# Optimization experiments

Hardware: AMD Instinct MI355X
Metric: run time of the kernel (lower is better)

The kernel has to match this reference:

```python
import jax, jax.numpy as jnp
import numpy as np

B, S, D = 1, 2048, 3072
H, DH = 24, 128
ENC, NIP = 512, 64
COND = (512 // 8) * (512 // 8) * 16 // 64  # 1024 cond tokens per lora
RANK, ALPHA, LW, IP_SCALE = 16, 16.0, 1.0, 1.0
EPS = 1e-5


def _rms(x):
    return x * jax.lax.rsqrt(jnp.mean(x * x, axis=-1, keepdims=True) + EPS)


def _to_heads(x):
    b, s, _ = x.shape
    return x.reshape(b, s, H, DH).transpose(0, 2, 1, 3)  # [B,H,S,DH]


def _from_heads(x):
    b, h, s, d = x.shape
    return x.transpose(0, 2, 1, 3).reshape(b, s, h * d)


def _lora(x, dn, up):
    # token mask keeps only the cond block (number=0, n_loras=1 -> last COND tokens)
    y = ((x[:, -COND:, :] @ dn) @ up) * (ALPHA / RANK)
    z = jnp.zeros((x.shape[0], x.shape[1] - COND, up.shape[1]), x.dtype)
    return jnp.concatenate([z, y], axis=1)


def _sdpa(q, k, v, mask=None):
    s = jnp.einsum('bhqd,bhkd->bhqk', q, k) * (1.0 / np.sqrt(DH))
    if mask is not None:
        s = s + mask
    return jnp.einsum('bhqk,bhkd->bhqd', jax.nn.softmax(s, axis=-1), v)


def _forward(hidden_states, encoder_hidden_states, image_emb,
             Wq, bq, Wk, bk, Wv, bv, Waq, baq, Wak, bak, Wav, bav,
             Wo, bo, Wao, bao, Wkip, Wvip,
             lq_dn, lq_up, lk_dn, lk_up, lv_dn, lv_up, lp_dn, lp_up):
    hs, ehs, img = hidden_states, encoder_hidden_states, image_emb
    # context (encoder) projections + RMSNorm on q/k
    eq = _rms(_to_heads(ehs @ Waq + baq))
    ek = _rms(_to_heads(ehs @ Wak + bak))
    ev = _to_heads(ehs @ Wav + bav)
    # main-stream q/k/v with masked LoRA branches
    q = hs @ Wq + bq + LW * _lora(hs, lq_dn, lq_up)
    k = hs @ Wk + bk + LW * _lora(hs, lk_dn, lk_up)
    v = hs @ Wv + bv + LW * _lora(hs, lv_dn, lv_up)
    q = _rms(_to_heads(q))
    k = _rms(_to_heads(k))
    v = _to_heads(v)
    # IP-adapter branch: extra K/V from image_emb, norm_added_k is RMSNorm(128)
    kip = _rms(_to_heads(img @ Wkip))
    vip = _to_heads(img @ Wvip)
    ip_out = _from_heads(_sdpa(q, kip, vip))  # [B,S,D]
    # concat encoder stream ahead of main stream
    q = jnp.concatenate([eq, q], axis=2)
    k = jnp.concatenate([ek, k], axis=2)
    v = jnp.concatenate([ev, v], axis=2)
    SL = ENC + S
    SB = SL - COND  # scaled_block_size
    m = jnp.ones((SL, SL), jnp.float32)
    m = m.at[:SB, :].set(0.0)        # non-cond rows attend everywhere
    m = m.at[SB:, SB:].set(0.0)      # single cond block attends to itself (n_loras=1)
    mask = m * (-1e20)
    out = _from_heads(_sdpa(q, k, v, mask))  # [B,SL,D]
    enc_out = out[:, :ENC, :]
    main = out[:, ENC:, :] + IP_SCALE * ip_out
    main = main @ Wo + bo
    main = main + LW * _lora(main, lp_dn, lp_up)  # proj LoRA (to_out dropout=identity)
    enc_out = enc_out @ Wao + bao
    return jnp.concatenate([enc_out, main], axis=1)  # [B, ENC+S, D]


def setup_inputs():
    key = jax.random.key(0)
    ks = iter(jax.random.split(key, 40))
    w = lambda *sh: jax.random.normal(next(ks), sh, jnp.float32) * 0.02
    return dict(
        hidden_states=jax.random.normal(next(ks), (B, S, D), jnp.float32),
        encoder_hidden_states=jax.random.normal(next(ks), (B, ENC, D), jnp.float32),
        image_emb=jax.random.normal(next(ks), (B, NIP, D), jnp.float32),
        Wq=w(D, D), bq=w(D), Wk=w(D, D), bk=w(D), Wv=w(D, D), bv=w(D),
        Waq=w(D, D), baq=w(D), Wak=w(D, D), bak=w(D), Wav=w(D, D), bav=w(D),
        Wo=w(D, D), bo=w(D), Wao=w(D, D), bao=w(D),
        Wkip=w(D, D), Wvip=w(D, D),
        lq_dn=w(D, RANK), lq_up=w(RANK, D), lk_dn=w(D, RANK), lk_up=w(RANK, D),
        lv_dn=w(D, RANK), lv_up=w(RANK, D), lp_dn=w(D, RANK), lp_up=w(RANK, D),
    )


def reference(hidden_states, encoder_hidden_states, image_emb,
              Wq, bq, Wk, bk, Wv, bv, Waq, baq, Wak, bak, Wav, bav,
              Wo, bo, Wao, bao, Wkip, Wvip,
              lq_dn, lq_up, lk_dn, lk_up, lv_dn, lv_up, lp_dn, lp_up):
    return _forward(hidden_states, encoder_hidden_states, image_emb,
                    Wq, bq, Wk, bk, Wv, bv, Waq, baq, Wak, bak, Wav, bav,
                    Wo, bo, Wao, bao, Wkip, Wvip,
                    lq_dn, lq_up, lk_dn, lk_up, lv_dn, lv_up, lp_dn, lp_up)
```

## Files before the change

### kernel.cpp

```cpp
#include <hip/hip_runtime.h>

typedef unsigned short u16;
typedef short s16x8 __attribute__((ext_vector_type(8)));
typedef float f32x4 __attribute__((ext_vector_type(4)));
typedef const __attribute__((address_space(1))) unsigned int* as1_u32p;
typedef __attribute__((address_space(3))) unsigned int* as3_u32p;

static_assert(sizeof(s16x8) == 16, "");

struct alignas(8) U16x4 { u16 x, y, z, w; };

__device__ __forceinline__ u16 f2bf(float f) {
  union { float f; unsigned u; } c; c.f = f;
  return (u16)((c.u + 0x7fffu + ((c.u >> 16) & 1u)) >> 16);
}
__device__ __forceinline__ float bf2f(u16 h) {
  union { unsigned u; float f; } c; c.u = ((unsigned)h) << 16;
  return c.f;
}
__device__ __forceinline__ void async16(const void* g, void* l) {
  __builtin_amdgcn_global_load_lds((as1_u32p)g, (as3_u32p)l, 16, 0, 0);
}

__launch_bounds__(256)
__global__ void mega_prep(const float* __restrict__ Waq, const float* __restrict__ Wak,
                          const float* __restrict__ Wav, const float* __restrict__ Wq,
                          const float* __restrict__ Wk, const float* __restrict__ Wv,
                          u16* __restrict__ WTbE, u16* __restrict__ WTbM,
                          const float* __restrict__ Wo, const float* __restrict__ bo,
                          const float* __restrict__ lp_dn, float* __restrict__ Wod,
                          const float* __restrict__ d0, const float* __restrict__ d1,
                          const float* __restrict__ d2, float* __restrict__ tl,
                          const float* __restrict__ hs, u16* __restrict__ hsb,
                          const float* __restrict__ ehs, u16* __restrict__ ehsb,
                          const float* __restrict__ img, u16* __restrict__ imgb,
                          const float* __restrict__ baq, const float* __restrict__ bak,
                          const float* __restrict__ bav, const float* __restrict__ bq,
                          const float* __restrict__ bk, const float* __restrict__ bv,
                          float* __restrict__ bpk,
                          const float* __restrict__ u0, const float* __restrict__ u1,
                          const float* __restrict__ u2) {
  __shared__ char lmem[4352];
  const int b = blockIdx.x;
  if (b < 55296) {
    int mat = b / 9216, tile = b % 9216;
    const float* src = (mat == 0) ? Waq : (mat == 1) ? Wak : (mat == 2) ? Wav
                       : (mat == 3) ? Wq : (mat == 4) ? Wk : Wv;
    u16* dst = (mat < 3) ? WTbE + (long)mat * 3072 * 3072
                         : WTbM + (long)(mat - 3) * 3072 * 3136;
    const int ldd = (mat < 3) ? 3072 : 3136;
    float (*tile2)[33] = (float(*)[33])lmem;
    int k0 = (tile / 96) * 32, n0 = (tile % 96) * 32;
    int r = threadIdx.x >> 3, c4 = (threadIdx.x & 7) * 4;
    float4 v = *(const float4*)(src + (long)(k0 + r) * 3072 + n0 + c4);
    tile2[r][c4 + 0] = v.x; tile2[r][c4 + 1] = v.y;
    tile2[r][c4 + 2] = v.z; tile2[r][c4 + 3] = v.w;
    __syncthreads();
    U16x4 o{f2bf(tile2[c4 + 0][r]), f2bf(tile2[c4 + 1][r]),
            f2bf(tile2[c4 + 2][r]), f2bf(tile2[c4 + 3][r])};
    *(U16x4*)(dst + (long)(n0 + r) * ldd + k0 + c4) = o;
  } else if (b < 56320) {
    const int m = b - 55296;
    float (*red)[48] = (float(*)[48])lmem;
    const float* xr = hs + (long)(1024 + m) * 3072;
    float p[48];
#pragma unroll
    for (int r = 0; r < 48; ++r) p[r] = 0.f;
    for (int k = threadIdx.x; k < 3072; k += 256) {
      float a = xr[k];
      const float* e0 = d0 + (long)k * 16;
      const float* e1 = d1 + (long)k * 16;
      const float* e2 = d2 + (long)k * 16;
#pragma unroll
      for (int r = 0; r < 16; ++r) {
        p[r]      += a * e0[r];
        p[16 + r] += a * e1[r];
        p[32 + r] += a * e2[r];
      }
    }
#pragma unroll
    for (int r = 0; r < 48; ++r)
#pragma unroll
      for (int st = 1; st < 64; st <<= 1) p[r] += __shfl_xor(p[r], st, 64);
    int lane = threadIdx.x & 63, w = threadIdx.x >> 6;
    if (lane == 0) {
#pragma unroll
      for (int r = 0; r < 48; ++r) red[w][r] = p[r];
    }
    __syncthreads();
    if (threadIdx.x < 48) {
      int r = threadIdx.x;
      tl[(long)m * 48 + r] = red[0][r] + red[1][r] + red[2][r] + red[3][r];
    }
  } else if (b < 59393) {
    const int m = b - 56320;
    float (*red)[16] = (float(*)[16])lmem;
    const float* xr = (m < 3072) ? Wo + (long)m * 3072 : bo;
    float p[16];
#pragma unroll
    for (int r = 0; r < 16; ++r) p[r] = 0.f;
    for (int k = threadIdx.x; k < 3072; k += 256) {
      float a = xr[k];
      const float* d = lp_dn + (long)k * 16;
#pragma unroll
      for (int r = 0; r < 16; ++r) p[r] += a * d[r];
    }
#pragma unroll
    for (int r = 0; r < 16; ++r)
#pragma unroll
      for (int st = 1; st < 64; st <<= 1) p[r] += __shfl_xor(p[r], st, 64);
    int lane = threadIdx.x & 63, w = threadIdx.x >> 6;
    if (lane == 0) {
#pragma unroll
      for (int r = 0; r < 16; ++r) red[w][r] = p[r];
    }
    __syncthreads();
    if (threadIdx.x < 16) {
      int r = threadIdx.x;
      Wod[(long)m * 16 + r] = red[0][r] + red[1][r] + red[2][r] + red[3][r];
    }
  } else {
    const int pb = b - 59393;
    if (pb < 3136) {
      long idx = (long)pb * 256 + threadIdx.x;
      long m = idx / 392, c = idx % 392;
      U16x4 o0{0, 0, 0, 0}, o1{0, 0, 0, 0};
      if (c < 384) {
        const float* p = hs + m * 3072 + c * 8;
        float4 a = *(const float4*)p;
        float4 bb = *(const float4*)(p + 4);
        o0 = U16x4{f2bf(a.x), f2bf(a.y), f2bf(a.z), f2bf(a.w)};
        o1 = U16x4{f2bf(bb.x), f2bf(bb.y), f2bf(bb.z), f2bf(bb.w)};
      }
      u16* d = hsb + m * 3136 + c * 8;
      *(U16x4*)d = o0;
      *(U16x4*)(d + 4) = o1;
    } else if (pb < 3904) {
      long i = ((long)(pb - 3136) * 256 + threadIdx.x) * 8;
      float4 a = *(const float4*)(ehs + i);
      float4 bb = *(const float4*)(ehs + i + 4);
      *(U16x4*)(ehsb + i) = U16x4{f2bf(a.x), f2bf(a.y), f2bf(a.z), f2bf(a.w)};
      *(U16x4*)(ehsb + i + 4) = U16x4{f2bf(bb.x), f2bf(bb.y), f2bf(bb.z), f2bf(bb.w)};
    } else if (pb < 4000) {
      long i = ((long)(pb - 3904) * 256 + threadIdx.x) * 8;
      float4 a = *(const float4*)(img + i);
      float4 bb = *(const float4*)(img + i + 4);
      *(U16x4*)(imgb + i) = U16x4{f2bf(a.x), f2bf(a.y), f2bf(a.z), f2bf(a.w)};
      *(U16x4*)(imgb + i + 4) = U16x4{f2bf(bb.x), f2bf(bb.y), f2bf(bb.z), f2bf(bb.w)};
    } else if (pb < 4072) {
      int i = (pb - 4000) * 256 + threadIdx.x;
      if (i < 9216)
        bpk[i] = (i < 3072) ? baq[i] : (i < 6144) ? bak[i - 3072] : bav[i - 6144];
      else {
        int j = i - 9216;
        bpk[i] = (j < 3072) ? bq[j] : (j < 6144) ? bk[j - 3072] : bv[j - 6144];
      }
    } else {
      int idx = (pb - 4072) * 256 + threadIdx.x;
      int n = idx >> 6, i = idx & 63;
      int seg = n / 3072;
      const float* up = (seg == 0) ? u0 : (seg == 1) ? u1 : u2;
      int r = i - seg * 16;
      float v = (r >= 0 && r < 16) ? up[(long)r * 3072 + (n - seg * 3072)] : 0.f;
      WTbM[(long)n * 3136 + 3072 + i] = f2bf(v);
    }
  }
}

__launch_bounds__(256)
__global__ void t_hs(const float* __restrict__ tl, u16* __restrict__ hsb) {
  int idx = blockIdx.x * 256 + threadIdx.x;
  int m = idx / 48, r = idx % 48;
  hsb[(long)(1024 + m) * 3136 + 3072 + r] = f2bf(tl[m * 48 + r]);
}

__launch_bounds__(256)
__global__ void transpose2(const float* __restrict__ Wkip, const float* __restrict__ Wvip,
                           u16* __restrict__ E1) {
  __shared__ float tile[32][33];
  const int b = blockIdx.x;
  int mat = b / 9216, t = b % 9216;
  const float* src = mat ? Wvip : Wkip;
  u16* dst = E1 + (long)mat * 3072 * 3072;
  int k0 = (t / 96) * 32, n0 = (t % 96) * 32;
  int r = threadIdx.x >> 3, c4 = (threadIdx.x & 7) * 4;
  float4 v = *(const float4*)(src + (long)(k0 + r) * 3072 + n0 + c4);
  tile[r][c4 + 0] = v.x; tile[r][c4 + 1] = v.y;
  tile[r][c4 + 2] = v.z; tile[r][c4 + 3] = v.w;
  __syncthreads();
  U16x4 o{f2bf(tile[c4 + 0][r]), f2bf(tile[c4 + 1][r]),
          f2bf(tile[c4 + 2][r]), f2bf(tile[c4 + 3][r])};
  *(U16x4*)(dst + (long)(n0 + r) * 3072 + k0 + c4) = o;
}

template <int BM, int MI, int NI>
__launch_bounds__(256)
__global__ void gemm_f32(const u16* __restrict__ A, int lda,
                         const u16* __restrict__ B, int ldb,
                         float* __restrict__ C, int ldc,
                         const float* __restrict__ bias, int KC, long cstride) {
  constexpr int WCOLS = 128 / (NI * 16);
  constexpr int ABYTES = BM * 128;
  __shared__ char smem[ABYTES + 128 * 128];
  char* As = smem;
  char* Bs = smem + ABYTES;
  const int tid = threadIdx.x;
  const int w = tid >> 6, lane = tid & 63;
  const int lr = lane & 15, lg = lane >> 4;
  const int wr = w / WCOLS, wc = w % WCOLS;
  const int nbx = gridDim.x;
  const int nwg = nbx * gridDim.y;
  const int flat = blockIdx.y * nbx + blockIdx.x;
  const int swz = (flat & 7) * (nwg >> 3) + (flat >> 3);
  const long m0 = (long)(swz % nbx) * BM;
  const long n0 = (long)(swz / nbx) * 128;
  const int k0 = blockIdx.z * KC;
  C += blockIdx.z * cstride;
  f32x4 acc[MI][NI] = {};
  constexpr int ACH = BM / 32;
  for (int kb = k0; kb < k0 + KC; kb += 64) {
    __syncthreads();
#pragma unroll
    for (int i = 0; i < ACH; ++i) {
      int x = (tid + 256 * i) * 16;
      int row = x >> 7;
      int sx = x ^ ((row & 7) << 4);
      async16((const char*)(A + (m0 + row) * lda + kb) + (sx & 127),
              As + ((w << 10) + (i << 12)));
    }
#pragma unroll
    for (int i = 0; i < 4; ++i) {
      int x = (tid + 256 * i) * 16;
      int row = x >> 7;
      int sx = x ^ ((row & 7) << 4);
      async16((const char*)(B + (n0 + row) * ldb + kb) + (sx & 127),
              Bs + ((w << 10) + (i << 12)));
    }
    __syncthreads();
#pragma unroll
    for (int kc = 0; kc < 2; ++kc) {
      s16x8 af[MI], bfr[NI];
#pragma unroll
      for (int mi = 0; mi < MI; ++mi) {
        int row = wr * (MI * 16) + mi * 16 + lr;
        int b = ((row << 7) + kc * 64 + lg * 16) ^ ((row & 7) << 4);
        af[mi] = *(const s16x8*)(As + b);
      }
#pragma unroll
      for (int ni = 0; ni < NI; ++ni) {
        int row = wc * (NI * 16) + ni * 16 + lr;
        int b = ((row << 7) + kc * 64 + lg * 16) ^ ((row & 7) << 4);
        bfr[ni] = *(const s16x8*)(Bs + b);
      }
#pragma unroll
      for (int mi = 0; mi < MI; ++mi)
#pragma unroll
        for (int ni = 0; ni < NI; ++ni)
          acc[mi][ni] = __builtin_amdgcn_mfma_f32_16x16x32_bf16(af[mi], bfr[ni], acc[mi][ni], 0, 0, 0);
    }
  }
#pragma unroll
  for (int mi = 0; mi < MI; ++mi) {
#pragma unroll
    for (int ni = 0; ni < NI; ++ni) {
      long col = n0 + wc * (NI * 16) + ni * 16 + lr;
      float bv = bias ? bias[col] : 0.f;
#pragma unroll
      for (int j = 0; j < 4; ++j) {
        long row = m0 + wr * (MI * 16) + mi * 16 + lg * 4 + j;
        C[row * ldc + col] = acc[mi][ni][j] + bv;
      }
    }
  }
}

__launch_bounds__(256)
__global__ void rms_ip(const float* __restrict__ in, u16* __restrict__ Ko,
                       u16* __restrict__ Vo) {
  const int t = blockIdx.x & 63;
  const int vhalf = blockIdx.x >> 6;
  const int col0 = vhalf ? 3072 : 0;
  u16* out = vhalf ? Vo : Ko;
  const int w = threadIdx.x >> 6, lane = threadIdx.x & 63;
  const long ps = 64LL * 6144;
#pragma unroll
  for (int hh = 0; hh < 6; ++hh) {
    int h = w * 6 + hh;
    const float* x = in + (long)t * 6144 + col0 + h * 128 + lane * 2;
    float a = x[0] + x[ps] + x[2 * ps] + x[3 * ps];
    float b = x[1] + x[1 + ps] + x[1 + 2 * ps] + x[1 + 3 * ps];
    float scale = 1.f;
    if (!vhalf) {
      float ss = a * a + b * b;
#pragma unroll
      for (int st = 1; st < 64; st <<= 1) ss += __shfl_xor(ss, st, 64);
      scale = rsqrtf(ss * (1.f / 128.f) + 1e-5f);
    }
    unsigned pa = f2bf(a * scale), pb = f2bf(b * scale);
    *(unsigned*)(out + ((long)h * 64 + t) * 128 + lane * 2) = pa | (pb << 16);
  }
}

__launch_bounds__(256)
__global__ void transpose_v(const u16* __restrict__ VB, u16* __restrict__ VT, int T) {
  __shared__ u16 tile[32][34];
  int h = blockIdx.z;
  int t0 = blockIdx.x * 32, d0 = blockIdx.y * 32;
  int r = threadIdx.x >> 3, c4 = (threadIdx.x & 7) * 4;
  U16x4 v = *(const U16x4*)(VB + ((long)h * T + t0 + r) * 128 + d0 + c4);
  tile[r][c4 + 0] = v.x; tile[r][c4 + 1] = v.y;
  tile[r][c4 + 2] = v.z; tile[r][c4 + 3] = v.w;
  __syncthreads();
  U16x4 o{tile[c4 + 0][r], tile[c4 + 1][r], tile[c4 + 2][r], tile[c4 + 3][r]};
  *(U16x4*)(VT + ((long)h * 128 + d0 + r) * T + t0 + c4) = o;
}

__launch_bounds__(256, 3)
__global__ void gemm_qkv(const u16* __restrict__ Aenc, const u16* __restrict__ Amain,
                         const u16* __restrict__ Benc, const u16* __restrict__ Bmain,
                         u16* __restrict__ Qo, u16* __restrict__ Ko, u16* __restrict__ VTo,
                         const float* __restrict__ bpk) {
  __shared__ char smem[32768];
  char* As = smem;
  char* Bs = smem + 16384;
  const int tid = threadIdx.x;
  const int w = tid >> 6, lane = tid & 63;
  const int lr = lane & 15, lg = lane >> 4;
  const int wr = w >> 1, wc = w & 1;
  const int flat = blockIdx.y * 20 + blockIdx.x;
  const int swz = (flat & 7) * 180 + (flat >> 3);
  const int mx = swz % 20;
  const long n0 = (long)(swz / 20) * 128;
  const u16* A;
  const u16* B;
  const float* bias;
  int lda, ldb, K, t0;
  long m0;
  if (mx < 4) {
    A = Aenc; lda = 3072; B = Benc; ldb = 3072; K = 3072; t0 = 0;
    m0 = (long)mx * 128; bias = bpk;
  } else {
    A = Amain; lda = 3136; B = Bmain; ldb = 3136; K = 3136; t0 = 512;
    m0 = (long)(mx - 4) * 128; bias = bpk + 9216;
  }
  f32x4 acc[4][4] = {};
  for (int kb = 0; kb < K; kb += 64) {
    __syncthreads();
#pragma unroll
    for (int i = 0; i < 4; ++i) {
      int x = (tid + 256 * i) * 16;
      int row = x >> 7;
      int sx = (x & 127) ^ ((row & 7) << 4);
      async16((const char*)(A + (m0 + row) * lda + kb) + sx, As + x);
    }
#pragma unroll
    for (int i = 0; i < 4; ++i) {
      int x = (tid + 256 * i) * 16;
      int row = x >> 7;
      int sx = (x & 127) ^ ((row & 7) << 4);
      async16((const char*)(B + (n0 + row) * ldb + kb) + sx, Bs + x);
    }
    __syncthreads();
#pragma unroll
    for (int kc = 0; kc < 2; ++kc) {
      s16x8 af[4], bfr[4];
#pragma unroll
      for (int mi = 0; mi < 4; ++mi) {
        int row = wr * 64 + mi * 16 + lr;
        af[mi] = *(const s16x8*)(As + (row << 7) + ((kc * 64 + lg * 16) ^ ((row & 7) << 4)));
      }
#pragma unroll
      for (int ni = 0; ni < 4; ++ni) {
        int row = wc * 64 + ni * 16 + lr;
        bfr[ni] = *(const s16x8*)(Bs + (row << 7) + ((kc * 64 + lg * 16) ^ ((row & 7) << 4)));
      }
#pragma unroll
      for (int mi = 0; mi < 4; ++mi)
#pragma unroll
        for (int ni = 0; ni < 4; ++ni)
          acc[mi][ni] = __builtin_amdgcn_mfma_f32_16x16x32_bf16(af[mi], bfr[ni], acc[mi][ni], 0, 0, 0);
    }
  }
  const int seg = (int)(n0 / 3072);
  const int head = (int)((n0 % 3072) >> 7);
#pragma unroll
  for (int ni = 0; ni < 4; ++ni) {
    float bv = bias[n0 + wc * 64 + ni * 16 + lr];
#pragma unroll
    for (int mi = 0; mi < 4; ++mi)
#pragma unroll
      for (int j = 0; j < 4; ++j) acc[mi][ni][j] += bv;
  }
  __syncthreads();
  float scl[4][4];
  if (seg < 2) {
    float* red = (float*)smem;
#pragma unroll
    for (int mi = 0; mi < 4; ++mi)
#pragma unroll
      for (int j = 0; j < 4; ++j) {
        float s = 0.f;
#pragma unroll
        for (int ni = 0; ni < 4; ++ni) s += acc[mi][ni][j] * acc[mi][ni][j];
#pragma unroll
        for (int st = 1; st < 16; st <<= 1) s += __shfl_xor(s, st, 16);
        if (lr == 0) red[(wr * 64 + mi * 16 + lg * 4 + j) * 2 + wc] = s;
        scl[mi][j] = s;
      }
    __syncthreads();
#pragma unroll
    for (int mi = 0; mi < 4; ++mi)
#pragma unroll
      for (int j = 0; j < 4; ++j) {
        int row = wr * 64 + mi * 16 + lg * 4 + j;
        float t = red[row * 2] + red[row * 2 + 1];
        scl[mi][j] = rsqrtf(t * (1.f / 128.f) + 1e-5f);
      }
    __syncthreads();
  }
  if (seg < 2) {
#pragma unroll
    for (int mi = 0; mi < 4; ++mi)
#pragma unroll
      for (int ni = 0; ni < 4; ++ni) {
        int d2 = (wc * 64 + ni * 16 + lr) * 2;
#pragma unroll
        for (int j = 0; j < 4; ++j) {
          int tok = wr * 64 + mi * 16 + lg * 4 + j;
          *(u16*)(smem + tok * 256 + (d2 ^ ((tok & 7) << 4))) =
              f2bf(acc[mi][ni][j] * scl[mi][j]);
        }
      }
  } else {
#pragma unroll
    for (int mi = 0; mi < 4; ++mi)
#pragma unroll
      for (int ni = 0; ni < 4; ++ni) {
        int d = wc * 64 + ni * 16 + lr;
        int tok0b = (wr * 64 + mi * 16 + lg * 4) * 2;
        U16x4 o{f2bf(acc[mi][ni][0]), f2bf(acc[mi][ni][1]),
                f2bf(acc[mi][ni][2]), f2bf(acc[mi][ni][3])};
        *(U16x4*)(smem + d * 256 + (tok0b ^ ((d & 7) << 4))) = o;
      }
  }
  __syncthreads();
#pragma unroll
  for (int i = 0; i < 8; ++i) {
    int x = (tid + 256 * i) * 16;
    int row = x >> 8, col = x & 255;
    s16x8 vdat = *(const s16x8*)(smem + row * 256 + (col ^ ((row & 7) << 4)));
    if (seg < 2) {
      u16* g = (seg == 0 ? Qo : Ko) + ((long)head * 2560 + t0 + m0 + row) * 128;
      *(s16x8*)((char*)g + col) = vdat;
    } else {
      u16* g = VTo + ((long)head * 128 + row) * 2560 + t0 + m0;
      *(s16x8*)((char*)g + col) = vdat;
    }
  }
}

__launch_bounds__(512, 2)
__global__ void attn_fused(const u16* __restrict__ QB, const u16* __restrict__ KB,
                           const u16* __restrict__ VT, const u16* __restrict__ KipB,
                           const u16* __restrict__ VipT, u16* __restrict__ OutTok) {
  __shared__ char smem[81920];
  const int bf = blockIdx.x;
  const int tid = threadIdx.x;
  const int w = tid >> 6, lane = tid & 63;
  const int lr = lane & 15, lg = lane >> 4;
  int h, qb;
  if (bf < 288) { h = bf / 12; qb = bf % 12; }
  else { int s = bf - 288; h = s / 8; qb = 12 + s % 8; }
  const int q0 = qb * 128;
  const bool ip = (q0 >= 512);
  const u16* Qrow = QB + (long)(h * 2560 + q0 + w * 16 + lr) * 128;
  s16x8 qf[4];
#pragma unroll
  for (int dc = 0; dc < 4; ++dc) qf[dc] = *(const s16x8*)(Qrow + dc * 32 + lg * 8);
  f32x4 accO[8] = {};
  float l_r[4] = {0.f, 0.f, 0.f, 0.f};
  const int kv0 = (q0 >= 1536) ? 1536 : 0;
  const float sc = 0.08838834764831845f;

  auto stage_main = [&](int kv, int buf) {
#pragma unroll
    for (int i = 0; i < 2; ++i) {
      int x = (tid + 512 * i) * 16;
      int row = x >> 8;
      int sx = x ^ ((row & 7) << 4);
      async16((const char*)(KB + (long)(h * 2560 + kv + row) * 128) + (sx & 255),
              smem + buf * 16384 + ((i << 13) + (w << 10)));
    }
#pragma unroll
    for (int i = 0; i < 2; ++i) {
      int x = (tid + 512 * i) * 16;
      int row = x >> 7;
      int sx = x ^ ((row & 7) << 4);
      async16((const char*)(VT + (long)(h * 128 + row) * 2560 + kv) + (sx & 127),
              smem + 32768 + buf * 16384 + ((i << 13) + (w << 10)));
    }
  };
  auto stage_ip = [&](int buf) {
#pragma unroll
    for (int i = 0; i < 2; ++i) {
      int x = (tid + 512 * i) * 16;
      int row = x >> 8;
      int sx = x ^ ((row & 7) << 4);
      async16((const char*)(KipB + (long)(h * 64 + row) * 128) + (sx & 255),
              smem + buf * 16384 + ((i << 13) + (w << 10)));
    }
#pragma unroll
    for (int i = 0; i < 2; ++i) {
      int x = (tid + 512 * i) * 16;
      int row = x >> 7;
      int sx = x ^ ((row & 7) << 4);
      async16((const char*)(VipT + (long)(h * 128 + row) * 64) + (sx & 127),
              smem + 32768 + buf * 16384 + ((i << 13) + (w << 10)));
    }
  };

  stage_main(kv0, 0);
  __syncthreads();
  int cur = 0;
  for (int kv = kv0; kv < 2560; kv += 64) {
    if (kv + 64 < 2560) stage_main(kv + 64, cur ^ 1);
    else if (ip) stage_ip(cur ^ 1);
    const char* Ks = smem + cur * 16384;
    const char* Vs = smem + 32768 + cur * 16384;
    char* Pw = smem + 65536 + w * 2048;
    f32x4 s[4] = {};
    __builtin_amdgcn_s_setprio(1);
#pragma unroll
    for (int kt = 0; kt < 4; ++kt)
#pragma unroll
      for (int dc = 0; dc < 4; ++dc) {
        int row = kt * 16 + lr;
        int b = ((row << 8) + dc * 64 + lg * 16) ^ ((row & 7) << 4);
        s16x8 kf = *(const s16x8*)(Ks + b);
        s[kt] = __builtin_amdgcn_mfma_f32_16x16x32_bf16(qf[dc], kf, s[kt], 0, 0, 0);
      }
    __builtin_amdgcn_s_setprio(0);
#pragma unroll
    for (int kt = 0; kt < 4; ++kt)
#pragma unroll
      for (int j = 0; j < 4; ++j) {
        float pv = __expf(fmaf(s[kt][j], sc, -12.0f));
        l_r[j] += pv;
        int prow = lg * 4 + j;
        int b = ((prow << 7) + (kt * 16 + lr) * 2) ^ ((prow & 7) << 4);
        *(u16*)(Pw + b) = f2bf(pv);
// ... 10 lines not shown
        int b = ((row << 7) + kc * 64 + lg * 16) ^ ((row & 7) << 4);
        s16x8 vf = *(const s16x8*)(Vs + b);
        accO[dt] = __builtin_amdgcn_mfma_f32_16x16x32_bf16(pf, vf, accO[dt], 0, 0, 0);
      }
    }
    __builtin_amdgcn_s_setprio(0);
    __syncthreads();
    cur ^= 1;
  }
#pragma unroll
  for (int j = 0; j < 4; ++j) {
#pragma unroll
    for (int st = 1; st < 16; st <<= 1) l_r[j] += __shfl_xor(l_r[j], st, 16);
    l_r[j] = 1.f / l_r[j];
  }
#pragma unroll
  for (int dt = 0; dt < 8; ++dt)
#pragma unroll
    for (int j = 0; j < 4; ++j) accO[dt][j] *= l_r[j];
  if (ip) {
    const char* Ks = smem + cur * 16384;
    const char* Vs = smem + 32768 + cur * 16384;
    char* Pw = smem + 65536 + w * 2048;
    f32x4 s2[4] = {};
#pragma unroll
    for (int kt = 0; kt < 4; ++kt)
#pragma unroll
      for (int dc = 0; dc < 4; ++dc) {
        int row = kt * 16 + lr;
        int b = ((row << 8) + dc * 64 + lg * 16) ^ ((row & 7) << 4);
        s16x8 kf = *(const s16x8*)(Ks + b);
        s2[kt] = __builtin_amdgcn_mfma_f32_16x16x32_bf16(qf[dc], kf, s2[kt], 0, 0, 0);
      }
    float p2[4][4];
    float l2[4] = {0.f, 0.f, 0.f, 0.f};
#pragma unroll
    for (int kt = 0; kt < 4; ++kt)
#pragma unroll
      for (int j = 0; j < 4; ++j) {
        float pv = __expf(fmaf(s2[kt][j], sc, -12.0f));
        p2[kt][j] = pv;
        l2[j] += pv;
      }
#pragma unroll
    for (int j = 0; j < 4; ++j) {
#pragma unroll
      for (int st = 1; st < 16; st <<= 1) l2[j] += __shfl_xor(l2[j], st, 16);
      l2[j] = 1.f / l2[j];
    }
#pragma unroll
    for (int kt = 0; kt < 4; ++kt)
#pragma unroll
      for (int j = 0; j < 4; ++j) {
        int prow = lg * 4 + j;
        int b = ((prow << 7) + (kt * 16 + lr) * 2) ^ ((prow & 7) << 4);
        *(u16*)(Pw + b) = f2bf(p2[kt][j] * l2[j]);
      }
    asm volatile("s_waitcnt lgkmcnt(0)" ::: "memory");
#pragma unroll
    for (int kc = 0; kc < 2; ++kc) {
      int pb = ((lr << 7) + kc * 64 + lg * 16) ^ ((lr & 7) << 4);
      s16x8 pf = *(const s16x8*)(Pw + pb);
#pragma unroll
      for (int dt = 0; dt < 8; ++dt) {
        int row = dt * 16 + lr;
        int b = ((row << 7) + kc * 64 + lg * 16) ^ ((row & 7) << 4);
        s16x8 vf = *(const s16x8*)(Vs + b);
        accO[dt] = __builtin_amdgcn_mfma_f32_16x16x32_bf16(pf, vf, accO[dt], 0, 0, 0);
      }
    }
  }
#pragma unroll
  for (int j = 0; j < 4; ++j) {
    long tok = q0 + w * 16 + lg * 4 + j;
#pragma unroll
    for (int dt = 0; dt < 8; ++dt) {
      long col = h * 128 + dt * 16 + lr;
      OutTok[tok * 3136 + col] = f2bf(accO[dt][j]);
    }
  }
}

__launch_bounds__(256)
__global__ void ttail_mega(u16* __restrict__ At, const float* __restrict__ Wod,
                           const float* __restrict__ Wao, const float* __restrict__ Wo,
                           u16* __restrict__ WTbE, u16* __restrict__ WTbM,
                           const float* __restrict__ lp_up) {
  __shared__ char lmem[4352];
  const int b = blockIdx.x;
  if (b < 18432) {
    int mat = b / 9216, tile = b % 9216;
    const float* src = mat ? Wo : Wao;
    u16* dst = mat ? WTbM : WTbE;
    const int ldd = mat ? 3136 : 3072;
    float (*tile2)[33] = (float(*)[33])lmem;
    int k0 = (tile / 96) * 32, n0 = (tile % 96) * 32;
    int r = threadIdx.x >> 3, c4 = (threadIdx.x & 7) * 4;
    float4 v = *(const float4*)(src + (long)(k0 + r) * 3072 + n0 + c4);
    tile2[r][c4 + 0] = v.x; tile2[r][c4 + 1] = v.y;
    tile2[r][c4 + 2] = v.z; tile2[r][c4 + 3] = v.w;
    __syncthreads();
    U16x4 o{f2bf(tile2[c4 + 0][r]), f2bf(tile2[c4 + 1][r]),
            f2bf(tile2[c4 + 2][r]), f2bf(tile2[c4 + 3][r])};
    *(U16x4*)(dst + (long)(n0 + r) * ldd + k0 + c4) = o;
  } else if (b < 19200) {
    int idx = (b - 18432) * 256 + threadIdx.x;
    int n = idx >> 6, i = idx & 63;
    float v = (i < 16) ? lp_up[(long)i * 3072 + n] : 0.f;
    WTbM[(long)n * 3136 + 3072 + i] = f2bf(v);
  } else {
    float (*red)[16] = (float(*)[16])lmem;
    const int tok = b - 19200;
    u16* tail = At + (long)(512 + tok) * 3136 + 3072;
    if (tok < 1024) {
      if (threadIdx.x < 64) tail[threadIdx.x] = 0;
      return;
    }
    const u16* xr = At + (long)(512 + tok) * 3136;
    float p[16];
#pragma unroll
    for (int r = 0; r < 16; ++r) p[r] = 0.f;
    for (int n = threadIdx.x; n < 3072; n += 256) {
      float a = bf2f(xr[n]);
      const float* wd = Wod + (long)n * 16;
#pragma unroll
      for (int r = 0; r < 16; ++r) p[r] += a * wd[r];
    }
#pragma unroll
    for (int r = 0; r < 16; ++r)
#pragma unroll
      for (int st = 1; st < 64; st <<= 1) p[r] += __shfl_xor(p[r], st, 64);
    int lane = threadIdx.x & 63, w = threadIdx.x >> 6;
    if (lane == 0) {
#pragma unroll
      for (int r = 0; r < 16; ++r) red[w][r] = p[r];
    }
    __syncthreads();
    if (threadIdx.x < 64) {
      if (threadIdx.x < 16) {
        int r = threadIdx.x;
        float t = red[0][r] + red[1][r] + red[2][r] + red[3][r] + Wod[3072L * 16 + r];
        tail[r] = f2bf(t);
      } else {
        tail[threadIdx.x] = 0;
      }
    }
  }
}

__launch_bounds__(256)
__global__ void gemm_out(const u16* __restrict__ Atok, const u16* __restrict__ Benc,
                         const u16* __restrict__ Bmain, float* __restrict__ outp,
                         const float* __restrict__ bao, const float* __restrict__ bo) {
  __shared__ char smem[128 * 128 + 128 * 128];
  char* As = smem;
  char* Bs = smem + 128 * 128;
  const int tid = threadIdx.x;
  const int w = tid >> 6, lane = tid & 63;
  const int lr = lane & 15, lg = lane >> 4;
  const int wr = w >> 1, wc = w & 1;
  const int flat = blockIdx.y * 20 + blockIdx.x;
  const int swz = (flat & 7) * 60 + (flat >> 3);
  const int mx = swz % 20;
  const long n0 = (long)(swz / 20) * 128;
  const u16* A;
  const u16* B;
  const float* bias;
  float* C;
  int ldb, K;
  long m0;
  if (mx < 4) {
    A = Atok; B = Benc; ldb = 3072; K = 3072; bias = bao; C = outp;
    m0 = (long)mx * 128;
  } else {
    A = Atok + 512L * 3136; B = Bmain; ldb = 3136; K = 3136; bias = bo;
    C = outp + 512L * 3072; m0 = (long)(mx - 4) * 128;
  }
  f32x4 acc[4][4] = {};
  for (int kb = 0; kb < K; kb += 64) {
    __syncthreads();
#pragma unroll
    for (int i = 0; i < 4; ++i) {
      int x = (tid + 256 * i) * 16;
      int row = x >> 7;
      int sx = x ^ ((row & 7) << 4);
      async16((const char*)(A + (m0 + row) * 3136 + kb) + (sx & 127),
              As + ((w << 10) + (i << 12)));
    }
#pragma unroll
    for (int i = 0; i < 4; ++i) {
      int x = (tid + 256 * i) * 16;
      int row = x >> 7;
      int sx = x ^ ((row & 7) << 4);
      async16((const char*)(B + (n0 + row) * ldb + kb) + (sx & 127),
              Bs + ((w << 10) + (i << 12)));
    }
    __syncthreads();
#pragma unroll
    for (int kc = 0; kc < 2; ++kc) {
      s16x8 af[4], bfr[4];
#pragma unroll
      for (int mi = 0; mi < 4; ++mi) {
        int row = wr * 64 + mi * 16 + lr;
        int b = ((row << 7) + kc * 64 + lg * 16) ^ ((row & 7) << 4);
        af[mi] = *(const s16x8*)(As + b);
      }
#pragma unroll
      for (int ni = 0; ni < 4; ++ni) {
        int row = wc * 64 + ni * 16 + lr;
        int b = ((row << 7) + kc * 64 + lg * 16) ^ ((row & 7) << 4);
        bfr[ni] = *(const s16x8*)(Bs + b);
      }
#pragma unroll
      for (int mi = 0; mi < 4; ++mi)
#pragma unroll
        for (int ni = 0; ni < 4; ++ni)
          acc[mi][ni] = __builtin_amdgcn_mfma_f32_16x16x32_bf16(af[mi], bfr[ni], acc[mi][ni], 0, 0, 0);
    }
  }
#pragma unroll
  for (int mi = 0; mi < 4; ++mi) {
#pragma unroll
    for (int ni = 0; ni < 4; ++ni) {
      long col = n0 + wc * 64 + ni * 16 + lr;
      float bv = bias[col];
#pragma unroll
      for (int j = 0; j < 4; ++j) {
        long row = m0 + wr * 64 + mi * 16 + lg * 4 + j;
        C[row * 3072 + col] = acc[mi][ni][j] + bv;
      }
    }
  }
}


extern "C" void kernel_launch(void* const* d_in, const int* in_sizes, int n_in,
                              void* d_out, int out_size, void* d_ws, size_t ws_size,
                              hipStream_t stream) {
  const float* hs    = (const float*)d_in[0];
  const float* ehs   = (const float*)d_in[1];
  const float* img   = (const float*)d_in[2];
  const float* Wq    = (const float*)d_in[3];
  const float* bq    = (const float*)d_in[4];
  const float* Wk    = (const float*)d_in[5];
  const float* bk    = (const float*)d_in[6];
  const float* Wv    = (const float*)d_in[7];
  const float* bv    = (const float*)d_in[8];
  const float* Waq   = (const float*)d_in[9];
  const float* baq   = (const float*)d_in[10];
  const float* Wak   = (const float*)d_in[11];
  const float* bak   = (const float*)d_in[12];
  const float* Wav   = (const float*)d_in[13];
  const float* bav   = (const float*)d_in[14];
  const float* Wo    = (const float*)d_in[15];
  const float* bo    = (const float*)d_in[16];
  const float* Wao   = (const float*)d_in[17];
  const float* bao   = (const float*)d_in[18];
  const float* Wkip  = (const float*)d_in[19];
  const float* Wvip  = (const float*)d_in[20];
  const float* lq_dn = (const float*)d_in[21];
  const float* lq_up = (const float*)d_in[22];
  const float* lk_dn = (const float*)d_in[23];
  const float* lk_up = (const float*)d_in[24];
  const float* lv_dn = (const float*)d_in[25];
  const float* lv_up = (const float*)d_in[26];
  const float* lp_dn = (const float*)d_in[27];
  const float* lp_up = (const float*)d_in[28];
  float* outp = (float*)d_out;

  char* ws = (char*)d_ws;
  size_t off = 0;
  auto take = [&](size_t b) { char* p = ws + off; off += (b + 255) & ~(size_t)255; return p; };
  u16*   WTbE = (u16*)take(3LL * 3072 * 3072 * 2);
  u16*   WTbM = (u16*)take(3LL * 3072 * 3136 * 2);
  u16*   hsb  = (u16*)take(2048LL * 3136 * 2);
  u16*   ehsb = (u16*)take(512LL * 3072 * 2);
  u16*   imgb = (u16*)take(64LL * 3072 * 2);
  u16*   VTf  = (u16*)take(24LL * 128 * 2560 * 2);
  float* IP0  = (float*)take(4LL * 64 * 6144 * 4);
  u16*   KipB = (u16*)take(24LL * 64 * 128 * 2);
  u16*   VipB = (u16*)take(24LL * 64 * 128 * 2);
  u16*   VipT = (u16*)take(24LL * 128 * 64 * 2);
  float* bpk  = (float*)take(2 * 9216 * 4);
  float* tl   = (float*)take(1024LL * 48 * 4);
  float* Wod  = (float*)take(3073LL * 16 * 4);
  u16* QBf = (u16*)d_out;
  u16* KBf = (u16*)d_out + 24LL * 2560 * 128;
  u16* AttnTok = hsb;
  u16* E1 = WTbE + 3072LL * 3072;

  mega_prep<<<65769, 256, 0, stream>>>(Waq, Wak, Wav, Wq, Wk, Wv, WTbE, WTbM,
                                       Wo, bo, lp_dn, Wod,
                                       lq_dn, lk_dn, lv_dn, tl,
                                       hs, hsb, ehs, ehsb, img, imgb,
                                       baq, bak, bav, bq, bk, bv, bpk,
                                       lq_up, lk_up, lv_up);
  t_hs<<<192, 256, 0, stream>>>(tl, hsb);

  gemm_qkv<<<dim3(20, 72), 256, 0, stream>>>(ehsb, hsb, WTbE, WTbM, QBf, KBf, VTf, bpk);

  transpose2<<<18432, 256, 0, stream>>>(Wkip, Wvip, E1);

  gemm_f32<64, 4, 2><<<dim3(1, 48, 4), 256, 0, stream>>>(imgb, 3072, E1, 3072, IP0, 6144,
                                                          nullptr, 768, 64LL * 6144);
  rms_ip<<<128, 256, 0, stream>>>(IP0, KipB, VipB);
  transpose_v<<<dim3(2, 4, 24), 256, 0, stream>>>(VipB, VipT, 64);

  attn_fused<<<480, 512, 0, stream>>>(QBf, KBf, VTf, KipB, VipT, AttnTok);

  ttail_mega<<<21248, 256, 0, stream>>>(AttnTok, Wod, Wao, Wo, WTbE, WTbM, lp_up);

  gemm_out<<<dim3(20, 24), 256, 0, stream>>>(AttnTok, WTbE, WTbM, outp, bao, bo);
}
```

Measured before the change: 599.8 us.

## Fold weight transposes into attention launch and compute IP projections directly from fp32

Each block of the weight-transpose code now handles four 32x32 tiles instead of one, which cuts the block count of the prep kernel. The IP-adapter K/V projection no longer transposes and converts Wkip/Wvip to bf16 before a GEMM. A simple FMA kernel reads the fp32 weights directly, rms_ip writes V already transposed, and the separate transpose_v is dropped. The Wo/Wao transposes and the lp_up tail now run as extra blocks appended to the attention kernel so they overlap with attention, and the token-tail reduction moves to its own kernel. The risk is that the scalar IP projection is slower than the MFMA GEMM, and that the extra blocks contend with attention for resources.

```diff
diff --git a/kernel.cpp b/kernel.cpp
--- a/kernel.cpp
+++ b/kernel.cpp
@@ -40,33 +40,43 @@
                           float* __restrict__ bpk,
                           const float* __restrict__ u0, const float* __restrict__ u1,
                           const float* __restrict__ u2) {
-  __shared__ char lmem[4352];
+  __shared__ char lmem[16896];
   const int b = blockIdx.x;
-  if (b < 55296) {
-    int mat = b / 9216, tile = b % 9216;
+  const int tid = threadIdx.x;
+  if (b < 13824) {
+    int mat = b / 2304, tile = b % 2304;
     const float* src = (mat == 0) ? Waq : (mat == 1) ? Wak : (mat == 2) ? Wav
                        : (mat == 3) ? Wq : (mat == 4) ? Wk : Wv;
     u16* dst = (mat < 3) ? WTbE + (long)mat * 3072 * 3072
                          : WTbM + (long)(mat - 3) * 3072 * 3136;
     const int ldd = (mat < 3) ? 3072 : 3136;
-    float (*tile2)[33] = (float(*)[33])lmem;
-    int k0 = (tile / 96) * 32, n0 = (tile % 96) * 32;
-    int r = threadIdx.x >> 3, c4 = (threadIdx.x & 7) * 4;
-    float4 v = *(const float4*)(src + (long)(k0 + r) * 3072 + n0 + c4);
-    tile2[r][c4 + 0] = v.x; tile2[r][c4 + 1] = v.y;
-    tile2[r][c4 + 2] = v.z; tile2[r][c4 + 3] = v.w;
-    __syncthreads();
-    U16x4 o{f2bf(tile2[c4 + 0][r]), f2bf(tile2[c4 + 1][r]),
-            f2bf(tile2[c4 + 2][r]), f2bf(tile2[c4 + 3][r])};
-    *(U16x4*)(dst + (long)(n0 + r) * ldd + k0 + c4) = o;
-  } else if (b < 56320) {
-    const int m = b - 55296;
+    float (*tile2)[32][33] = (float(*)[32][33])lmem;
+    int k0 = (tile / 96) * 128, n0 = (tile % 96) * 32;
+    int r = tid >> 3, c4 = (tid & 7) * 4;
+    float4 v[4];
+#pragma unroll
+    for (int t = 0; t < 4; ++t)
+      v[t] = *(const float4*)(src + (long)(k0 + 32 * t + r) * 3072 + n0 + c4);
+#pragma unroll
+    for (int t = 0; t < 4; ++t) {
+      tile2[t][r][c4 + 0] = v[t].x; tile2[t][r][c4 + 1] = v[t].y;
+      tile2[t][r][c4 + 2] = v[t].z; tile2[t][r][c4 + 3] = v[t].w;
+    }
+    __syncthreads();
+#pragma unroll
+    for (int t = 0; t < 4; ++t) {
+      U16x4 o{f2bf(tile2[t][c4 + 0][r]), f2bf(tile2[t][c4 + 1][r]),
+              f2bf(tile2[t][c4 + 2][r]), f2bf(tile2[t][c4 + 3][r])};
+      *(U16x4*)(dst + (long)(n0 + r) * ldd + k0 + 32 * t + c4) = o;
+    }
+  } else if (b < 14848) {
+    const int m = b - 13824;
     float (*red)[48] = (float(*)[48])lmem;
     const float* xr = hs + (long)(1024 + m) * 3072;
     float p[48];
 #pragma unroll
     for (int r = 0; r < 48; ++r) p[r] = 0.f;
-    for (int k = threadIdx.x; k < 3072; k += 256) {
+    for (int k = tid; k < 3072; k += 256) {
       float a = xr[k];
       const float* e0 = d0 + (long)k * 16;
       const float* e1 = d1 + (long)k * 16;
@@ -82,24 +92,24 @@
     for (int r = 0; r < 48; ++r)
 #pragma unroll
       for (int st = 1; st < 64; st <<= 1) p[r] += __shfl_xor(p[r], st, 64);
-    int lane = threadIdx.x & 63, w = threadIdx.x >> 6;
+    int lane = tid & 63, w = tid >> 6;
     if (lane == 0) {
 #pragma unroll
       for (int r = 0; r < 48; ++r) red[w][r] = p[r];
     }
     __syncthreads();
-    if (threadIdx.x < 48) {
-      int r = threadIdx.x;
+    if (tid < 48) {
+      int r = tid;
       tl[(long)m * 48 + r] = red[0][r] + red[1][r] + red[2][r] + red[3][r];
     }
-  } else if (b < 59393) {
-    const int m = b - 56320;
+  } else if (b < 17921) {
+    const int m = b - 14848;
     float (*red)[16] = (float(*)[16])lmem;
     const float* xr = (m < 3072) ? Wo + (long)m * 3072 : bo;
     float p[16];
 #pragma unroll
     for (int r = 0; r < 16; ++r) p[r] = 0.f;
-    for (int k = threadIdx.x; k < 3072; k += 256) {
+    for (int k = tid; k < 3072; k += 256) {
       float a = xr[k];
       const float* d = lp_dn + (long)k * 16;
 #pragma unroll
@@ -109,20 +119,20 @@
     for (int r = 0; r < 16; ++r)
 #pragma unroll
       for (int st = 1; st < 64; st <<= 1) p[r] += __shfl_xor(p[r], st, 64);
-    int lane = threadIdx.x & 63, w = threadIdx.x >> 6;
+    int lane = tid & 63, w = tid >> 6;
     if (lane == 0) {
 #pragma unroll
       for (int r = 0; r < 16; ++r) red[w][r] = p[r];
     }
     __syncthreads();
-    if (threadIdx.x < 16) {
-      int r = threadIdx.x;
+    if (tid < 16) {
+      int r = tid;
       Wod[(long)m * 16 + r] = red[0][r] + red[1][r] + red[2][r] + red[3][r];
     }
   } else {
-    const int pb = b - 59393;
+    const int pb = b - 17921;
     if (pb < 3136) {
-      long idx = (long)pb * 256 + threadIdx.x;
+      long idx = (long)pb * 256 + tid;
       long m = idx / 392, c = idx % 392;
       U16x4 o0{0, 0, 0, 0}, o1{0, 0, 0, 0};
       if (c < 384) {
@@ -136,19 +146,19 @@
       *(U16x4*)d = o0;
       *(U16x4*)(d + 4) = o1;
     } else if (pb < 3904) {
-      long i = ((long)(pb - 3136) * 256 + threadIdx.x) * 8;
+      long i = ((long)(pb - 3136) * 256 + tid) * 8;
       float4 a = *(const float4*)(ehs + i);
       float4 bb = *(const float4*)(ehs + i + 4);
       *(U16x4*)(ehsb + i) = U16x4{f2bf(a.x), f2bf(a.y), f2bf(a.z), f2bf(a.w)};
       *(U16x4*)(ehsb + i + 4) = U16x4{f2bf(bb.x), f2bf(bb.y), f2bf(bb.z), f2bf(bb.w)};
     } else if (pb < 4000) {
-      long i = ((long)(pb - 3904) * 256 + threadIdx.x) * 8;
+      long i = ((long)(pb - 3904) * 256 + tid) * 8;
       float4 a = *(const float4*)(img + i);
       float4 bb = *(const float4*)(img + i + 4);
       *(U16x4*)(imgb + i) = U16x4{f2bf(a.x), f2bf(a.y), f2bf(a.z), f2bf(a.w)};
       *(U16x4*)(imgb + i + 4) = U16x4{f2bf(bb.x), f2bf(bb.y), f2bf(bb.z), f2bf(bb.w)};
     } else if (pb < 4072) {
-      int i = (pb - 4000) * 256 + threadIdx.x;
+      int i = (pb - 4000) * 256 + tid;
       if (i < 9216)
         bpk[i] = (i < 3072) ? baq[i] : (i < 6144) ? bak[i - 3072] : bav[i - 6144];
       else {
@@ -156,7 +166,7 @@
         bpk[i] = (j < 3072) ? bq[j] : (j < 6144) ? bk[j - 3072] : bv[j - 6144];
       }
     } else {
-      int idx = (pb - 4072) * 256 + threadIdx.x;
+      int idx = (pb - 4072) * 256 + tid;
       int n = idx >> 6, i = idx & 63;
       int seg = n / 3072;
       const float* up = (seg == 0) ? u0 : (seg == 1) ? u1 : u2;
@@ -175,112 +185,36 @@
 }
 
 __launch_bounds__(256)
-__global__ void transpose2(const float* __restrict__ Wkip, const float* __restrict__ Wvip,
-                           u16* __restrict__ E1) {
-  __shared__ float tile[32][33];
-  const int b = blockIdx.x;
-  int mat = b / 9216, t = b % 9216;
-  const float* src = mat ? Wvip : Wkip;
-  u16* dst = E1 + (long)mat * 3072 * 3072;
-  int k0 = (t / 96) * 32, n0 = (t % 96) * 32;
-  int r = threadIdx.x >> 3, c4 = (threadIdx.x & 7) * 4;
-  float4 v = *(const float4*)(src + (long)(k0 + r) * 3072 + n0 + c4);
-  tile[r][c4 + 0] = v.x; tile[r][c4 + 1] = v.y;
-  tile[r][c4 + 2] = v.z; tile[r][c4 + 3] = v.w;
-  __syncthreads();
-  U16x4 o{f2bf(tile[c4 + 0][r]), f2bf(tile[c4 + 1][r]),
-          f2bf(tile[c4 + 2][r]), f2bf(tile[c4 + 3][r])};
-  *(U16x4*)(dst + (long)(n0 + r) * 3072 + k0 + c4) = o;
-}
-
-template <int BM, int MI, int NI>
-__launch_bounds__(256)
-__global__ void gemm_f32(const u16* __restrict__ A, int lda,
-                         const u16* __restrict__ B, int ldb,
-                         float* __restrict__ C, int ldc,
-                         const float* __restrict__ bias, int KC, long cstride) {
-  constexpr int WCOLS = 128 / (NI * 16);
-  constexpr int ABYTES = BM * 128;
-  __shared__ char smem[ABYTES + 128 * 128];
-  char* As = smem;
-  char* Bs = smem + ABYTES;
-  const int tid = threadIdx.x;
-  const int w = tid >> 6, lane = tid & 63;
-  const int lr = lane & 15, lg = lane >> 4;
-  const int wr = w / WCOLS, wc = w % WCOLS;
-  const int nbx = gridDim.x;
-  const int nwg = nbx * gridDim.y;
-  const int flat = blockIdx.y * nbx + blockIdx.x;
-  const int swz = (flat & 7) * (nwg >> 3) + (flat >> 3);
-  const long m0 = (long)(swz % nbx) * BM;
-  const long n0 = (long)(swz / nbx) * 128;
-  const int k0 = blockIdx.z * KC;
-  C += blockIdx.z * cstride;
-  f32x4 acc[MI][NI] = {};
-  constexpr int ACH = BM / 32;
-  for (int kb = k0; kb < k0 + KC; kb += 64) {
-    __syncthreads();
-#pragma unroll
-    for (int i = 0; i < ACH; ++i) {
-      int x = (tid + 256 * i) * 16;
-      int row = x >> 7;
-      int sx = x ^ ((row & 7) << 4);
-      async16((const char*)(A + (m0 + row) * lda + kb) + (sx & 127),
-              As + ((w << 10) + (i << 12)));
-    }
-#pragma unroll
-    for (int i = 0; i < 4; ++i) {
-      int x = (tid + 256 * i) * 16;
-      int row = x >> 7;
-      int sx = x ^ ((row & 7) << 4);
-      async16((const char*)(B + (n0 + row) * ldb + kb) + (sx & 127),
-              Bs + ((w << 10) + (i << 12)));
-    }
-    __syncthreads();
-#pragma unroll
-    for (int kc = 0; kc < 2; ++kc) {
-      s16x8 af[MI], bfr[NI];
-#pragma unroll
-      for (int mi = 0; mi < MI; ++mi) {
-        int row = wr * (MI * 16) + mi * 16 + lr;
-        int b = ((row << 7) + kc * 64 + lg * 16) ^ ((row & 7) << 4);
-        af[mi] = *(const s16x8*)(As + b);
-      }
-#pragma unroll
-      for (int ni = 0; ni < NI; ++ni) {
-        int row = wc * (NI * 16) + ni * 16 + lr;
-        int b = ((row << 7) + kc * 64 + lg * 16) ^ ((row & 7) << 4);
-        bfr[ni] = *(const s16x8*)(Bs + b);
-      }
-#pragma unroll
-      for (int mi = 0; mi < MI; ++mi)
-#pragma unroll
-        for (int ni = 0; ni < NI; ++ni)
-          acc[mi][ni] = __builtin_amdgcn_mfma_f32_16x16x32_bf16(af[mi], bfr[ni], acc[mi][ni], 0, 0, 0);
-    }
-  }
-#pragma unroll
-  for (int mi = 0; mi < MI; ++mi) {
-#pragma unroll
-    for (int ni = 0; ni < NI; ++ni) {
-      long col = n0 + wc * (NI * 16) + ni * 16 + lr;
-      float bv = bias ? bias[col] : 0.f;
-#pragma unroll
-      for (int j = 0; j < 4; ++j) {
-        long row = m0 + wr * (MI * 16) + mi * 16 + lg * 4 + j;
-        C[row * ldc + col] = acc[mi][ni][j] + bv;
-      }
-    }
-  }
+__global__ void ip_direct(const u16* __restrict__ imgb, const float* __restrict__ Wkip,
+                          const float* __restrict__ Wvip, float* __restrict__ IP0) {
+  const int n0 = blockIdx.x * 32;
+  const int k0 = blockIdx.y * 768;
+  const int c = threadIdx.x & 31, g = threadIdx.x >> 5;
+  const float* W = (n0 < 3072) ? (Wkip + n0 + c) : (Wvip + (n0 - 3072) + c);
+  const u16* ib = imgb + (long)(g * 8) * 3072;
+  float acc[8] = {};
+  for (int k = k0; k < k0 + 768; k += 2) {
+    float w0 = W[(long)k * 3072];
+    float w1 = W[(long)(k + 1) * 3072];
+#pragma unroll
+    for (int j = 0; j < 8; ++j) {
+      unsigned pv = *(const unsigned*)(ib + (long)j * 3072 + k);
+      acc[j] = fmaf(bf2f((u16)(pv & 0xffff)), w0, acc[j]);
+      acc[j] = fmaf(bf2f((u16)(pv >> 16)), w1, acc[j]);
+    }
+  }
+  float* out = IP0 + (long)blockIdx.y * 64 * 6144;
+#pragma unroll
+  for (int j = 0; j < 8; ++j)
+    out[(long)(g * 8 + j) * 6144 + n0 + c] = acc[j];
 }
 
 __launch_bounds__(256)
 __global__ void rms_ip(const float* __restrict__ in, u16* __restrict__ Ko,
-                       u16* __restrict__ Vo) {
+                       u16* __restrict__ VipT) {
   const int t = blockIdx.x & 63;
   const int vhalf = blockIdx.x >> 6;
   const int col0 = vhalf ? 3072 : 0;
-  u16* out = vhalf ? Vo : Ko;
   const int w = threadIdx.x >> 6, lane = threadIdx.x & 63;
   const long ps = 64LL * 6144;
 #pragma unroll
@@ -289,30 +223,18 @@
     const float* x = in + (long)t * 6144 + col0 + h * 128 + lane * 2;
     float a = x[0] + x[ps] + x[2 * ps] + x[3 * ps];
     float b = x[1] + x[1 + ps] + x[1 + 2 * ps] + x[1 + 3 * ps];
-    float scale = 1.f;
     if (!vhalf) {
       float ss = a * a + b * b;
 #pragma unroll
       for (int st = 1; st < 64; st <<= 1) ss += __shfl_xor(ss, st, 64);
-      scale = rsqrtf(ss * (1.f / 128.f) + 1e-5f);
-    }
-    unsigned pa = f2bf(a * scale), pb = f2bf(b * scale);
-    *(unsigned*)(out + ((long)h * 64 + t) * 128 + lane * 2) = pa | (pb << 16);
-  }
-}
-
-__launch_bounds__(256)
-__global__ void transpose_v(const u16* __restrict__ VB, u16* __restrict__ VT, int T) {
-  __shared__ u16 tile[32][34];
-  int h = blockIdx.z;
-  int t0 = blockIdx.x * 32, d0 = blockIdx.y * 32;
-  int r = threadIdx.x >> 3, c4 = (threadIdx.x & 7) * 4;
-  U16x4 v = *(const U16x4*)(VB + ((long)h * T + t0 + r) * 128 + d0 + c4);
-  tile[r][c4 + 0] = v.x; tile[r][c4 + 1] = v.y;
-  tile[r][c4 + 2] = v.z; tile[r][c4 + 3] = v.w;
-  __syncthreads();
-  U16x4 o{tile[c4 + 0][r], tile[c4 + 1][r], tile[c4 + 2][r], tile[c4 + 3][r]};
-  *(U16x4*)(VT + ((long)h * 128 + d0 + r) * T + t0 + c4) = o;
+      float scale = rsqrtf(ss * (1.f / 128.f) + 1e-5f);
+      unsigned pa = f2bf(a * scale), pb = f2bf(b * scale);
+      *(unsigned*)(Ko + ((long)h * 64 + t) * 128 + lane * 2) = pa | (pb << 16);
+    } else {
+      VipT[((long)h * 128 + lane * 2) * 64 + t] = f2bf(a);
+      VipT[((long)h * 128 + lane * 2 + 1) * 64 + t] = f2bf(b);
+    }
+  }
 }
 
 __launch_bounds__(256, 3)
@@ -460,12 +382,50 @@
 }
 
 __launch_bounds__(512, 2)
-__global__ void attn_fused(const u16* __restrict__ QB, const u16* __restrict__ KB,
-                           const u16* __restrict__ VT, const u16* __restrict__ KipB,
-                           const u16* __restrict__ VipT, u16* __restrict__ OutTok) {
+__global__ void attn_mega(const u16* __restrict__ QB, const u16* __restrict__ KB,
+                          const u16* __restrict__ VT, const u16* __restrict__ KipB,
+                          const u16* __restrict__ VipT, u16* __restrict__ OutTok,
+                          const float* __restrict__ Wao, const float* __restrict__ Wo,
+                          u16* __restrict__ WTbE, u16* __restrict__ WTbM,
+                          const float* __restrict__ lp_up) {
   __shared__ char smem[81920];
   const int bf = blockIdx.x;
   const int tid = threadIdx.x;
+  if (bf >= 480) {
+    if (bf < 2784) {
+      int t2 = (bf - 480) * 2 + (tid >> 8);
+      int mat = t2 / 2304, tile = t2 % 2304;
+      const float* src = mat ? Wo : Wao;
+      u16* dst = mat ? WTbM : WTbE;
+      const int ldd = mat ? 3136 : 3072;
+      float (*tl4)[4][32][33] = (float(*)[4][32][33])smem;
+      int half = tid >> 8, lt = tid & 255;
+      int k0 = (tile / 96) * 128, n0t = (tile % 96) * 32;
+      int r = lt >> 3, c4 = (lt & 7) * 4;
+      float4 v[4];
+#pragma unroll
+      for (int t = 0; t < 4; ++t)
+        v[t] = *(const float4*)(src + (long)(k0 + 32 * t + r) * 3072 + n0t + c4);
+#pragma unroll
+      for (int t = 0; t < 4; ++t) {
+        tl4[half][t][r][c4 + 0] = v[t].x; tl4[half][t][r][c4 + 1] = v[t].y;
+        tl4[half][t][r][c4 + 2] = v[t].z; tl4[half][t][r][c4 + 3] = v[t].w;
+      }
+      __syncthreads();
+#pragma unroll
+      for (int t = 0; t < 4; ++t) {
+        U16x4 o{f2bf(tl4[half][t][c4 + 0][r]), f2bf(tl4[half][t][c4 + 1][r]),
+                f2bf(tl4[half][t][c4 + 2][r]), f2bf(tl4[half][t][c4 + 3][r])};
+        *(U16x4*)(dst + (long)(n0t + r) * ldd + k0 + 32 * t + c4) = o;
+      }
+    } else {
+      int idx = (bf - 2784) * 512 + tid;
+      int n = idx >> 6, i = idx & 63;
+      float v = (i < 16) ? lp_up[(long)i * 3072 + n] : 0.f;
+      WTbM[(long)n * 3136 + 3072 + i] = f2bf(v);
+    }
+    return;
+  }
   const int w = tid >> 6, lane = tid & 63;
   const int lr = lane & 15, lg = lane >> 4;
   int h, qb;
@@ -642,68 +602,41 @@
 }
 
 __launch_bounds__(256)
-__global__ void ttail_mega(u16* __restrict__ At, const float* __restrict__ Wod,
-                           const float* __restrict__ Wao, const float* __restrict__ Wo,
-                           u16* __restrict__ WTbE, u16* __restrict__ WTbM,
-                           const float* __restrict__ lp_up) {
-  __shared__ char lmem[4352];
-  const int b = blockIdx.x;
-  if (b < 18432) {
-    int mat = b / 9216, tile = b % 9216;
-    const float* src = mat ? Wo : Wao;
-    u16* dst = mat ? WTbM : WTbE;
-    const int ldd = mat ? 3136 : 3072;
-    float (*tile2)[33] = (float(*)[33])lmem;
-    int k0 = (tile / 96) * 32, n0 = (tile % 96) * 32;
-    int r = threadIdx.x >> 3, c4 = (threadIdx.x & 7) * 4;
-    float4 v = *(const float4*)(src + (long)(k0 + r) * 3072 + n0 + c4);
-    tile2[r][c4 + 0] = v.x; tile2[r][c4 + 1] = v.y;
-    tile2[r][c4 + 2] = v.z; tile2[r][c4 + 3] = v.w;
-    __syncthreads();
-    U16x4 o{f2bf(tile2[c4 + 0][r]), f2bf(tile2[c4 + 1][r]),
-            f2bf(tile2[c4 + 2][r]), f2bf(tile2[c4 + 3][r])};
-    *(U16x4*)(dst + (long)(n0 + r) * ldd + k0 + c4) = o;
-  } else if (b < 19200) {
-    int idx = (b - 18432) * 256 + threadIdx.x;
-    int n = idx >> 6, i = idx & 63;
-    float v = (i < 16) ? lp_up[(long)i * 3072 + n] : 0.f;
-    WTbM[(long)n * 3136 + 3072 + i] = f2bf(v);
-  } else {
-    float (*red)[16] = (float(*)[16])lmem;
-    const int tok = b - 19200;
-    u16* tail = At + (long)(512 + tok) * 3136 + 3072;
-    if (tok < 1024) {
-      if (threadIdx.x < 64) tail[threadIdx.x] = 0;
-      return;
-    }
-    const u16* xr = At + (long)(512 + tok) * 3136;
-    float p[16];
-#pragma unroll
-    for (int r = 0; r < 16; ++r) p[r] = 0.f;
-    for (int n = threadIdx.x; n < 3072; n += 256) {
-      float a = bf2f(xr[n]);
-      const float* wd = Wod + (long)n * 16;
-#pragma unroll
-      for (int r = 0; r < 16; ++r) p[r] += a * wd[r];
-    }
-#pragma unroll
-    for (int r = 0; r < 16; ++r)
-#pragma unroll
-      for (int st = 1; st < 64; st <<= 1) p[r] += __shfl_xor(p[r], st, 64);
-    int lane = threadIdx.x & 63, w = threadIdx.x >> 6;
-    if (lane == 0) {
-#pragma unroll
-      for (int r = 0; r < 16; ++r) red[w][r] = p[r];
-    }
-    __syncthreads();
-    if (threadIdx.x < 64) {
-      if (threadIdx.x < 16) {
-        int r = threadIdx.x;
-        float t = red[0][r] + red[1][r] + red[2][r] + red[3][r] + Wod[3072L * 16 + r];
-        tail[r] = f2bf(t);
-      } else {
-        tail[threadIdx.x] = 0;
-      }
+__global__ void t_tail(u16* __restrict__ At, const float* __restrict__ Wod) {
+  __shared__ float red[4][16];
+  const int tok = blockIdx.x;
+  u16* tail = At + (long)(512 + tok) * 3136 + 3072;
+  if (tok < 1024) {
+    if (threadIdx.x < 64) tail[threadIdx.x] = 0;
+    return;
+  }
+  const u16* xr = At + (long)(512 + tok) * 3136;
+  float p[16];
+#pragma unroll
+  for (int r = 0; r < 16; ++r) p[r] = 0.f;
+  for (int n = threadIdx.x; n < 3072; n += 256) {
+    float a = bf2f(xr[n]);
+    const float* wd = Wod + (long)n * 16;
+#pragma unroll
+    for (int r = 0; r < 16; ++r) p[r] += a * wd[r];
+  }
+#pragma unroll
+  for (int r = 0; r < 16; ++r)
+#pragma unroll
+    for (int st = 1; st < 64; st <<= 1) p[r] += __shfl_xor(p[r], st, 64);
+  int lane = threadIdx.x & 63, w = threadIdx.x >> 6;
+  if (lane == 0) {
+#pragma unroll
+    for (int r = 0; r < 16; ++r) red[w][r] = p[r];
+  }
+  __syncthreads();
+  if (threadIdx.x < 64) {
+    if (threadIdx.x < 16) {
+      int r = threadIdx.x;
+      float t = red[0][r] + red[1][r] + red[2][r] + red[3][r] + Wod[3072L * 16 + r];
+      tail[r] = f2bf(t);
+    } else {
+      tail[threadIdx.x] = 0;
     }
   }
 }
@@ -839,7 +772,6 @@
   u16*   VTf  = (u16*)take(24LL * 128 * 2560 * 2);
   float* IP0  = (float*)take(4LL * 64 * 6144 * 4);
   u16*   KipB = (u16*)take(24LL * 64 * 128 * 2);
-  u16*   VipB = (u16*)take(24LL * 64 * 128 * 2);
   u16*   VipT = (u16*)take(24LL * 128 * 64 * 2);
   float* bpk  = (float*)take(2 * 9216 * 4);
   float* tl   = (float*)take(1024LL * 48 * 4);
@@ -847,9 +779,8 @@
   u16* QBf = (u16*)d_out;
   u16* KBf = (u16*)d_out + 24LL * 2560 * 128;
   u16* AttnTok = hsb;
-  u16* E1 = WTbE + 3072LL * 3072;
-
-  mega_prep<<<65769, 256, 0, stream>>>(Waq, Wak, Wav, Wq, Wk, Wv, WTbE, WTbM,
+
+  mega_prep<<<24297, 256, 0, stream>>>(Waq, Wak, Wav, Wq, Wk, Wv, WTbE, WTbM,
                                        Wo, bo, lp_dn, Wod,
                                        lq_dn, lk_dn, lv_dn, tl,
                                        hs, hsb, ehs, ehsb, img, imgb,
@@ -859,16 +790,14 @@
 
   gemm_qkv<<<dim3(20, 72), 256, 0, stream>>>(ehsb, hsb, WTbE, WTbM, QBf, KBf, VTf, bpk);
 
-  transpose2<<<18432, 256, 0, stream>>>(Wkip, Wvip, E1);
-
-  gemm_f32<64, 4, 2><<<dim3(1, 48, 4), 256, 0, stream>>>(imgb, 3072, E1, 3072, IP0, 6144,
-                                                          nullptr, 768, 64LL * 6144);
-  rms_ip<<<128, 256, 0, stream>>>(IP0, KipB, VipB);
-  transpose_v<<<dim3(2, 4, 24), 256, 0, stream>>>(VipB, VipT, 64);
-
-  attn_fused<<<480, 512, 0, stream>>>(QBf, KBf, VTf, KipB, VipT, AttnTok);
-
-  ttail_mega<<<21248, 256, 0, stream>>>(AttnTok, Wod, Wao, Wo, WTbE, WTbM, lp_up);
+  ip_direct<<<dim3(192, 4), 256, 0, stream>>>(imgb, Wkip, Wvip, IP0);
+
+  rms_ip<<<128, 256, 0, stream>>>(IP0, KipB, VipT);
+
+  attn_mega<<<3168, 512, 0, stream>>>(QBf, KBf, VTf, KipB, VipT, AttnTok,
+                                      Wao, Wo, WTbE, WTbM, lp_up);
+
+  t_tail<<<2048, 256, 0, stream>>>(AttnTok, Wod);
 
   gemm_out<<<dim3(20, 24), 256, 0, stream>>>(AttnTok, WTbE, WTbM, outp, bao, bo);
 }
```

New measurement: 743.4 us. 1.24x slower.
